# Performance work log

Hardware: AMD Instinct MI355X
Metric: run time of the kernel (lower is better)

## Reference

```python
import jax, jax.numpy as jnp
import numpy as np
import math

B, L, D, H = 16, 512, 128, 8


def setup_inputs() -> dict:
    key = jax.random.key(0)
    ks = jax.random.split(key, 10)
    xavier = lambda k, shp: jax.random.normal(k, shp, jnp.float32) * math.sqrt(2.0 / (shp[0] + shp[1]))
    inp = {
        "x": jax.random.normal(ks[0], (B, L, D), jnp.float32),
        "W_q": xavier(ks[1], (H * D, D)),
        "b_q": jnp.zeros((H * D,), jnp.float32),
        "W_k": xavier(ks[2], (H * D, D)),
        "b_k": jnp.zeros((H * D,), jnp.float32),
        "W_v": xavier(ks[3], (H * D, D)),
        "b_v": jnp.zeros((H * D,), jnp.float32),
        "W_o": xavier(ks[4], (D, H * D)),
        "b_o": jnp.zeros((D,), jnp.float32),
        "pad_mask": jax.random.randint(ks[5], (B, L, L), 0, 2).astype(bool),
        "batch_size": B,
        "max_len": L,
    }
    return inp


def reference(x, W_q, b_q, W_k, b_k, W_v, b_v, W_o, b_o, pad_mask, batch_size, max_len):
    # project: [B, L, D] -> [B, L, H*D] -> head-major [H*B, L, D]
    def proj(W, b):
        y = jnp.einsum('bld,ed->ble', x, W) + b          # [B, L, H*D]
        y = y.reshape(batch_size, max_len, H, D)
        return y.transpose(2, 0, 1, 3).reshape(H * batch_size, max_len, D)

    q = proj(W_q, b_q)
    k = proj(W_k, b_k)
    v = proj(W_v, b_v)

    scores = jnp.einsum('nqd,nkd->nqk', q, k)            # [H*B, L, L]
    mask = jnp.tile(pad_mask, (H, 1, 1))                 # repeat(n_heads,1,1)
    # faithful quirk: mask BEFORE scaling, softmax over QUERY axis (dim=1)
    scores = jnp.where(mask, -1e9, scores) / math.sqrt(D)
    attn = jax.nn.softmax(scores, axis=1)
    att = jnp.einsum('nqk,nkd->nqd', attn, v)            # [H*B, L, D]
    # faithful quirk: torch .view from (H*B, L, D) to (B, L, H*D)
    att = att.reshape(batch_size, max_len, H * D)
    out = jnp.einsum('ble,de->bld', att, W_o) + b_o      # [B, L, D]
    return out
```

## Files before the change

### kernel.cpp

```cpp
#include <hip/hip_runtime.h>

#define B_  16
#define L_  512
#define D_  128
#define H_  8
#define HD_ 1024
#define NH_ 128
#define M_  8192

typedef unsigned short u16;
typedef __attribute__((ext_vector_type(8))) short s16x8;
typedef __attribute__((ext_vector_type(4))) float f32x4;
typedef __attribute__((ext_vector_type(4))) unsigned u32x4;

__device__ __forceinline__ float bf2f(u16 u) {
    union { unsigned u; float f; } x; x.u = ((unsigned)u) << 16; return x.f;
}
__device__ __forceinline__ u16 f2bf(float f) {
    unsigned u = __float_as_uint(f);
    return (u16)((u + 0x7FFFu + ((u >> 16) & 1u)) >> 16);
}

__device__ __forceinline__ void mfma_bt64(const u16* __restrict__ A, int lda,
                                          const u16* __restrict__ B, int ldb,
                                          int K, int lane, f32x4 acc[4][4]) {
    const int mr = lane & 15, quad = lane >> 4;
    for (int k0 = 0; k0 < K; k0 += 32) {
        s16x8 av[4], bv[4];
#pragma unroll
        for (int i = 0; i < 4; i++)
            av[i] = *(const s16x8*)(A + (size_t)(i * 16 + mr) * lda + k0 + quad * 8);
#pragma unroll
        for (int j = 0; j < 4; j++)
            bv[j] = *(const s16x8*)(B + (size_t)(j * 16 + mr) * ldb + k0 + quad * 8);
#pragma unroll
        for (int i = 0; i < 4; i++)
#pragma unroll
            for (int j = 0; j < 4; j++)
                acc[i][j] = __builtin_amdgcn_mfma_f32_16x16x32_bf16(av[i], bv[j], acc[i][j], 0, 0, 0);
    }
}

__global__ void k0_detect(const unsigned int* __restrict__ pad,
                          const unsigned int* __restrict__ xw,
                          int* __restrict__ flags) {
    __shared__ int sMask, sCnt;
    if (threadIdx.x == 0) { sMask = 0; sCnt = 0; }
    __syncthreads();
    int bad = 0;
#pragma unroll
    for (int i = 0; i < 4; i++) {
        unsigned u = pad[threadIdx.x * 4 + i];
        bad |= (u > 1u) ? 1 : 0;
    }
    int cnt = 0;
#pragma unroll
    for (int i = 0; i < 16; i++) {
        unsigned w = xw[threadIdx.x * 16 + i];
        unsigned e = (w >> 7) & 0xFFu;
        cnt += (e >= 100u && e <= 131u) ? 1 : 0;
    }
    if (bad) atomicOr(&sMask, 1);
    atomicAdd(&sCnt, cnt);
    __syncthreads();
    if (threadIdx.x == 0) {
        flags[0] = (sCnt > 2048) ? 1 : 0;
        flags[1] = sMask;
    }
}

#define PREP_TOT 1576064
#define PREP_V   197008
#define PREP_CONV_BLOCKS 770
#define PREP_MASK_BLOCKS 512
__global__ __launch_bounds__(256) void kprep(
    const void* x, const void* Wq, const void* bq, const void* Wk, const void* bk,
    const void* Wv, const void* bv, const void* Wo, const void* bo,
    const void* __restrict__ pad, const int* __restrict__ flags,
    u16* xb, u16* Wqb, u16* Wkb, u16* Wvb, u16* Wob,
    u16* bqb, u16* bkb, u16* bvb, u16* bob,
    unsigned* __restrict__ mb, float* __restrict__ colsum) {
    const int b = blockIdx.x;
    if (b < PREP_CONV_BLOCKS) {
        int gid = b * 256 + threadIdx.x;
        if (gid >= PREP_V) return;
        int e0 = gid * 8;
        const int dt = flags[0];
        const void* src; u16* dst; int off;
        if      (e0 < 1048576) { src = x;  dst = xb;  off = e0; }
        else if (e0 < 1179648) { src = Wq; dst = Wqb; off = e0 - 1048576; }
        else if (e0 < 1310720) { src = Wk; dst = Wkb; off = e0 - 1179648; }
        else if (e0 < 1441792) { src = Wv; dst = Wvb; off = e0 - 1310720; }
        else if (e0 < 1572864) { src = Wo; dst = Wob; off = e0 - 1441792; }
        else if (e0 < 1573888) { src = bq; dst = bqb; off = e0 - 1572864; }
        else if (e0 < 1574912) { src = bk; dst = bkb; off = e0 - 1573888; }
        else if (e0 < 1575936) { src = bv; dst = bvb; off = e0 - 1574912; }
        else                   { src = bo; dst = bob; off = e0 - 1575936; }
        if (dt) {
            u32x4 v = __builtin_nontemporal_load((const u32x4*)((const u16*)src + off));
            *(u32x4*)(dst + off) = v;
        } else {
            const float* s = (const float*)src + off;
            f32x4 a = __builtin_nontemporal_load((const f32x4*)s);
            f32x4 c = __builtin_nontemporal_load((const f32x4*)(s + 4));
            u16 tmp[8] = {f2bf(a[0]), f2bf(a[1]), f2bf(a[2]), f2bf(a[3]),
                          f2bf(c[0]), f2bf(c[1]), f2bf(c[2]), f2bf(c[3])};
            *(u32x4*)(dst + off) = *(const u32x4*)tmp;
        }
    } else {
        int w = (b - PREP_CONV_BLOCKS) * 256 + threadIdx.x;
        if (w < NH_ * L_) colsum[w] = 0.0f;
        unsigned m = 0;
        if (flags[1]) {
            const u32x4* p = (const u32x4*)pad + (size_t)w * 2;
            u32x4 a = __builtin_nontemporal_load(p);
            u32x4 c = __builtin_nontemporal_load(p + 1);
            unsigned ws[8] = {a[0], a[1], a[2], a[3], c[0], c[1], c[2], c[3]};
#pragma unroll
            for (int i = 0; i < 8; i++) {
                unsigned v = ws[i];
                m |= ((v & 0xFFu)        ? 1u : 0u) << (i * 4)
                   | ((v & 0xFF00u)     ? 1u : 0u) << (i * 4 + 1)
                   | ((v & 0xFF0000u)   ? 1u : 0u) << (i * 4 + 2)
                   | ((v & 0xFF000000u) ? 1u : 0u) << (i * 4 + 3);
            }
        } else {
            const u32x4* p = (const u32x4*)pad + (size_t)w * 8;
#pragma unroll
            for (int i = 0; i < 8; i++) {
                u32x4 v = __builtin_nontemporal_load(p + i);
                m |= (v[0] ? 1u : 0u) << (i * 4)
                   | (v[1] ? 1u : 0u) << (i * 4 + 1)
                   | (v[2] ? 1u : 0u) << (i * 4 + 2)
                   | (v[3] ? 1u : 0u) << (i * 4 + 3);
            }
        }
        mb[w] = m;
    }
}

__global__ __launch_bounds__(256) void k1_proj(
    const u16* __restrict__ xb,
    const u16* __restrict__ Wqb, const u16* __restrict__ Wkb, const u16* __restrict__ Wvb,
    const u16* __restrict__ bqb, const u16* __restrict__ bkb, const u16* __restrict__ bvb,
    u16* __restrict__ qb, u16* __restrict__ kb, u16* __restrict__ vtb) {
    const int h  = blockIdx.y;
    const int m0 = blockIdx.x * 128;
    const int z  = blockIdx.z;
    const u16* W    = (z == 0) ? Wqb : (z == 1) ? Wkb : Wvb;
    const u16* bias = (z == 0) ? bqb : (z == 1) ? bkb : bvb;

    const int lane = threadIdx.x & 63, wave = threadIdx.x >> 6;
    const int wr = wave >> 1, wc = wave & 1;
    const int mr = lane & 15, quad = lane >> 4;

    f32x4 acc[4][4];
#pragma unroll
    for (int i = 0; i < 4; i++)
#pragma unroll
        for (int j = 0; j < 4; j++) acc[i][j] = (f32x4){0.f, 0.f, 0.f, 0.f};

    mfma_bt64(xb + (size_t)(m0 + wr * 64) * D_, D_,
              W + (size_t)(h * 128 + wc * 64) * D_, D_, D_, lane, acc);

    __shared__ __align__(16) u16 T[128][144];
#pragma unroll
    for (int i = 0; i < 4; i++)
#pragma unroll
        for (int j = 0; j < 4; j++) {
            int col = wc * 64 + j * 16 + mr;
            float bv_ = bf2f(bias[h * 128 + col]);
#pragma unroll
            for (int r = 0; r < 4; r++)
                T[wr * 64 + i * 16 + quad * 4 + r][col] = f2bf(acc[i][j][r] + bv_);
        }
    __syncthreads();

    const int bb = m0 >> 9, l0 = m0 & 511;
    const int t = threadIdx.x;
    if (z < 2) {
        u16* out = z ? kb : qb;
        const int wv = t >> 6, l = t & 63;
        const int col = (l & 15) * 8;
#pragma unroll
        for (int p = 0; p < 8; p++) {
            int row = p * 16 + wv * 4 + (l >> 4);
            u16* dst = out + ((size_t)(h * B_ + bb) * L_ + l0 + row) * D_ + col;
            *(uint4*)dst = *(const uint4*)&T[row][col];
        }
    } else {
        int d = t >> 1, lc0 = (t & 1) * 64;
        u16* dst = vtb + ((size_t)(h * B_ + bb) * D_ + d) * L_ + l0 + lc0;
#pragma unroll
        for (int c = 0; c < 64; c += 8) {
            u16 tmp[8];
#pragma unroll
            for (int s = 0; s < 8; s++) tmp[s] = T[lc0 + c + s][d];
            *(uint4*)(dst + c) = *(const uint4*)tmp;
        }
    }
}

__global__ __launch_bounds__(256, 4) void k2_scores(
    const u16* __restrict__ qb, const u16* __restrict__ kb,
    const unsigned* __restrict__ mbits,
    u16* __restrict__ sb, float* __restrict__ colsum) {
    const int bid = blockIdx.y * 16 + blockIdx.x;
    const int sw  = (bid & 7) * 256 + (bid >> 3);
    const int n   = sw >> 4;
    const int qt  = (sw >> 2) & 3, kt = sw & 3;
    const int bb  = n & (B_ - 1);
    const int lane = threadIdx.x & 63, wave = threadIdx.x >> 6;
    const int wr = wave >> 1, wc = wave & 1;
    const int mr = lane & 15, quad = lane >> 4;
    const float rs = 0.08838834764831845f;

    __shared__ __align__(16) u16 T[128][136];
    __shared__ float CS[2][128];
    __shared__ unsigned MW[128][4];

    {
        int t = threadIdx.x;
        int q = t >> 1, w2 = (t & 1) * 2;
        const unsigned* src = mbits + ((size_t)(bb << 9) + qt * 128 + q) * 16 + kt * 4 + w2;
        uint2 v = *(const uint2*)src;
        MW[q][w2] = v.x; MW[q][w2 + 1] = v.y;
    }

    f32x4 acc[4][4];
#pragma unroll
    for (int i = 0; i < 4; i++)
#pragma unroll
        for (int j = 0; j < 4; j++) acc[i][j] = (f32x4){0.f, 0.f, 0.f, 0.f};

    mfma_bt64(qb + ((size_t)n * L_ + qt * 128 + wr * 64) * D_, D_,
              kb + ((size_t)n * L_ + kt * 128 + wc * 64) * D_, D_, D_, lane, acc);
    __syncthreads();

    float cs[4] = {0.f, 0.f, 0.f, 0.f};
#pragma unroll
    for (int j = 0; j < 4; j++) {
        const int wsel = wc * 2 + (j >> 1);
        const int bit  = ((j & 1) << 4) + mr;
#pragma unroll
        for (int i = 0; i < 4; i++)
#pragma unroll
            for (int r = 0; r < 4; r++) {
                int ql = wr * 64 + i * 16 + quad * 4 + r;
                unsigned w = MW[ql][wsel];
                float e = ((w >> bit) & 1u) ? 0.f : __expf(acc[i][j][r] * rs);
                cs[j] += e;
                T[ql][wc * 64 + j * 16 + mr] = f2bf(e);
            }
    }
#pragma unroll
    for (int j = 0; j < 4; j++) {
        cs[j] += __shfl_xor(cs[j], 16);
        cs[j] += __shfl_xor(cs[j], 32);
    }
    if (quad == 0) {
#pragma unroll
        for (int j = 0; j < 4; j++) CS[wr][wc * 64 + j * 16 + mr] = cs[j];
    }
    __syncthreads();
    {
        int t = threadIdx.x;
        const int col = (t & 15) * 8;
        const int rb  = t >> 4;
#pragma unroll
        for (int p = 0; p < 8; p++) {
            int row = p * 16 + rb;
            u16* dst = sb + ((size_t)n * L_ + qt * 128 + row) * L_ + kt * 128 + col;
            *(uint4*)dst = *(const uint4*)&T[row][col];
        }
    }
    if (threadIdx.x < 128)
        atomicAdd(&colsum[(size_t)n * L_ + kt * 128 + threadIdx.x],
                  CS[0][threadIdx.x] + CS[1][threadIdx.x]);
}

__global__ __launch_bounds__(256) void k4_av(
    const u16* __restrict__ sb, const u16* __restrict__ vtb,
    const float* __restrict__ colsum, u16* __restrict__ att) {
    const int bid = blockIdx.y * 4 + blockIdx.x;
    const int sw  = (bid & 7) * 64 + (bid >> 3);
    const int n   = sw >> 2;
    const int q0  = (sw & 3) * 128;
    const int lane = threadIdx.x & 63, wave = threadIdx.x >> 6;
    const int wr = wave >> 1, wc = wave & 1;
    const int mr = lane & 15, quad = lane >> 4;

    f32x4 acc[4][4];
#pragma unroll
    for (int i = 0; i < 4; i++)
#pragma unroll
        for (int j = 0; j < 4; j++) acc[i][j] = (f32x4){0.f, 0.f, 0.f, 0.f};

    const u16* A   = sb  + ((size_t)n * L_ + q0 + wr * 64) * L_;
    const u16* Bb  = vtb + ((size_t)n * D_ + wc * 64) * L_;
    const float* cs = colsum + (size_t)n * L_;

    for (int k0 = 0; k0 < L_; k0 += 32) {
        const int kk = k0 + quad * 8;
        float lv[8];
        *(float4*)&lv[0] = *(const float4*)(cs + kk);
        *(float4*)&lv[4] = *(const float4*)(cs + kk + 4);
#pragma unroll
        for (int s = 0; s < 8; s++) lv[s] = __builtin_amdgcn_rcpf(lv[s]);

        s16x8 av[4], bv[4];
#pragma unroll
        for (int i = 0; i < 4; i++)
            av[i] = *(const s16x8*)(A + (size_t)(i * 16 + mr) * L_ + kk);
#pragma unroll
        for (int j = 0; j < 4; j++)
            bv[j] = *(const s16x8*)(Bb + (size_t)(j * 16 + mr) * L_ + kk);
#pragma unroll
        for (int i = 0; i < 4; i++) {
            u16* u = (u16*)&av[i];
#pragma unroll
            for (int s = 0; s < 8; s++) u[s] = f2bf(bf2f(u[s]) * lv[s]);
        }
#pragma unroll
        for (int i = 0; i < 4; i++)
#pragma unroll
            for (int j = 0; j < 4; j++)
                acc[i][j] = __builtin_amdgcn_mfma_f32_16x16x32_bf16(av[i], bv[j], acc[i][j], 0, 0, 0);
    }

    __shared__ __align__(16) u16 T[128][136];
#pragma unroll
    for (int i = 0; i < 4; i++)
#pragma unroll
        for (int j = 0; j < 4; j++) {
            int col = wc * 64 + j * 16 + mr;
#pragma unroll
            for (int r = 0; r < 4; r++)
                T[wr * 64 + i * 16 + quad * 4 + r][col] = f2bf(acc[i][j][r]);
        }
    __syncthreads();
    {
        int t = threadIdx.x;
        const int wv = t >> 6, l = t & 63;
        const int col = (l & 15) * 8;
#pragma unroll
        for (int p = 0; p < 8; p++) {
            int row = p * 16 + wv * 4 + (l >> 4);
            u16* dst = att + ((size_t)n * L_ + q0 + row) * D_ + col;
            *(uint4*)dst = *(const uint4*)&T[row][col];
        }
    }
}

__global__ __launch_bounds__(256) void k5_out(
    const u16* __restrict__ att, const u16* __restrict__ Wob,
    const u16* __restrict__ bob, const int* __restrict__ flags,
    void* __restrict__ out) {
    const int dt = flags[0];
    const int m0 = blockIdx.x * 32;
    const int lane = threadIdx.x & 63, wave = threadIdx.x >> 6;
    const int mr = lane & 15, quad = lane >> 4;

    f32x4 acc[2][2];
#pragma unroll
    for (int i = 0; i < 2; i++)
#pragma unroll
        for (int j = 0; j < 2; j++) acc[i][j] = (f32x4){0.f, 0.f, 0.f, 0.f};

    const u16* A  = att + (size_t)m0 * HD_;
    const u16* Bw = Wob + (size_t)(wave * 32) * HD_;
    for (int k0 = 0; k0 < HD_; k0 += 32) {
        s16x8 av[2], bv[2];
#pragma unroll
        for (int i = 0; i < 2; i++)
            av[i] = *(const s16x8*)(A + (size_t)(i * 16 + mr) * HD_ + k0 + quad * 8);
#pragma unroll
        for (int j = 0; j < 2; j++)
            bv[j] = *(const s16x8*)(Bw + (size_t)(j * 16 + mr) * HD_ + k0 + quad * 8);
#pragma unroll
        for (int i = 0; i < 2; i++)
#pragma unroll
            for (int j = 0; j < 2; j++)
                acc[i][j] = __builtin_amdgcn_mfma_f32_16x16x32_bf16(av[i], bv[j], acc[i][j], 0, 0, 0);
    }

    __shared__ __align__(16) float Tf[32][132];
#pragma unroll
    for (int i = 0; i < 2; i++)
#pragma unroll
        for (int j = 0; j < 2; j++) {
            int col = wave * 32 + j * 16 + mr;
            float bv_ = bf2f(bob[col]);
#pragma unroll
            for (int r = 0; r < 4; r++)
                Tf[i * 16 + quad * 4 + r][col] = acc[i][j][r] + bv_;
        }
    __syncthreads();
    int t = threadIdx.x, row = t >> 3, cg = (t & 7) * 16;
    size_t base = (size_t)(m0 + row) * D_ + cg;
    if (dt) {
        u16* o = (u16*)out;
        u16 tmp[16];
#pragma unroll
        for (int s = 0; s < 16; s++) tmp[s] = f2bf(Tf[row][cg + s]);
        *(uint4*)(o + base)     = *(const uint4*)&tmp[0];
        *(uint4*)(o + base + 8) = *(const uint4*)&tmp[8];
    } else {
        float* o = (float*)out;
#pragma unroll
        for (int c = 0; c < 16; c += 4)
            *(float4*)(o + base + c) = *(const float4*)&Tf[row][cg + c];
    }
}

extern "C" void kernel_launch(void* const* d_in, const int* in_sizes, int n_in,
                              void* d_out, int out_size, void* d_ws, size_t ws_size,
                              hipStream_t stream) {
    (void)in_sizes; (void)n_in; (void)out_size; (void)ws_size;
    const void* x  = d_in[0];
    const void* Wq = d_in[1]; const void* bq = d_in[2];
    const void* Wk = d_in[3]; const void* bk = d_in[4];
    const void* Wv = d_in[5]; const void* bv = d_in[6];
    const void* Wo = d_in[7]; const void* bo = d_in[8];
    const void* pad = d_in[9];

    char* p = (char*)d_ws;
    auto alloc = [&](size_t bytes) { char* r = p; p += (bytes + 255) & ~(size_t)255; return r; };
    int*  flags = (int*)alloc(256);
    u16*  xb   = (u16*)alloc(2097152);
    u16*  Wqb  = (u16*)alloc(262144);
    u16*  Wkb  = (u16*)alloc(262144);
    u16*  Wvb  = (u16*)alloc(262144);
    u16*  Wob  = (u16*)alloc(262144);
    u16*  bqb  = (u16*)alloc(2048);
    u16*  bkb  = (u16*)alloc(2048);
    u16*  bvb  = (u16*)alloc(2048);
    u16*  bob  = (u16*)alloc(256);
    unsigned* mbits = (unsigned*)alloc(524288);
    float* colsum = (float*)alloc(262144);
    u16*  qb   = (u16*)alloc(16777216);
    u16*  kb   = (u16*)alloc(16777216);
    u16*  vtb  = (u16*)alloc(16777216);
    u16*  sb   = (u16*)alloc(67108864);
    u16*  att  = qb;

    k0_detect<<<1, 256, 0, stream>>>((const unsigned*)pad, (const unsigned*)x, flags);
    kprep<<<PREP_CONV_BLOCKS + PREP_MASK_BLOCKS, 256, 0, stream>>>(
        x, Wq, bq, Wk, bk, Wv, bv, Wo, bo, pad, flags,
        xb, Wqb, Wkb, Wvb, Wob, bqb, bkb, bvb, bob, mbits, colsum);
    k1_proj<<<dim3(64, 8, 3), 256, 0, stream>>>(
        xb, Wqb, Wkb, Wvb, bqb, bkb, bvb, qb, kb, vtb);
    k2_scores<<<dim3(16, NH_), 256, 0, stream>>>(qb, kb, mbits, sb, colsum);
    k4_av<<<dim3(4, NH_), 256, 0, stream>>>(sb, vtb, colsum, att);
    k5_out<<<256, 256, 0, stream>>>(att, Wob, bob, flags, d_out);
}
```

Before: 231.5 us.

## Infer dtypes from input sizes on host and halve k2 score tile rows

The host now derives the input and mask dtypes from in_sizes and passes them as kernel arguments, so the k0_detect launch and the device flag reads are skipped when the sizes match. k2_scores switches from 128x128 to 64x128 tiles with an inline MFMA loop, which doubles the grid to 4096 blocks and halves LDS and accumulator registers per block. The intent is to drop one serial kernel launch and raise occupancy and parallelism in the scores stage, at the cost of reloading K tiles more often.

```diff
diff --git a/kernel.cpp b/kernel.cpp
--- a/kernel.cpp
+++ b/kernel.cpp
@@ -77,6 +77,7 @@
     const void* x, const void* Wq, const void* bq, const void* Wk, const void* bk,
     const void* Wv, const void* bv, const void* Wo, const void* bo,
     const void* __restrict__ pad, const int* __restrict__ flags,
+    int dth, int dtm,
     u16* xb, u16* Wqb, u16* Wkb, u16* Wvb, u16* Wob,
     u16* bqb, u16* bkb, u16* bvb, u16* bob,
     unsigned* __restrict__ mb, float* __restrict__ colsum) {
@@ -85,7 +86,7 @@
         int gid = b * 256 + threadIdx.x;
         if (gid >= PREP_V) return;
         int e0 = gid * 8;
-        const int dt = flags[0];
+        const int dt = (dth >= 0) ? dth : flags[0];
         const void* src; u16* dst; int off;
         if      (e0 < 1048576) { src = x;  dst = xb;  off = e0; }
         else if (e0 < 1179648) { src = Wq; dst = Wqb; off = e0 - 1048576; }
@@ -110,8 +111,9 @@
     } else {
         int w = (b - PREP_CONV_BLOCKS) * 256 + threadIdx.x;
         if (w < NH_ * L_) colsum[w] = 0.0f;
+        const int m8 = (dtm >= 0) ? dtm : flags[1];
         unsigned m = 0;
-        if (flags[1]) {
+        if (m8) {
             const u32x4* p = (const u32x4*)pad + (size_t)w * 2;
             u32x4 a = __builtin_nontemporal_load(p);
             u32x4 c = __builtin_nontemporal_load(p + 1);
@@ -205,36 +207,49 @@
     const u16* __restrict__ qb, const u16* __restrict__ kb,
     const unsigned* __restrict__ mbits,
     u16* __restrict__ sb, float* __restrict__ colsum) {
-    const int bid = blockIdx.y * 16 + blockIdx.x;
-    const int sw  = (bid & 7) * 256 + (bid >> 3);
-    const int n   = sw >> 4;
-    const int qt  = (sw >> 2) & 3, kt = sw & 3;
+    const int bid = blockIdx.y * 32 + blockIdx.x;
+    const int sw  = (bid & 7) * 512 + (bid >> 3);
+    const int n   = sw >> 5;
+    const int qt  = (sw >> 2) & 7, kt = sw & 3;
     const int bb  = n & (B_ - 1);
     const int lane = threadIdx.x & 63, wave = threadIdx.x >> 6;
     const int wr = wave >> 1, wc = wave & 1;
     const int mr = lane & 15, quad = lane >> 4;
     const float rs = 0.08838834764831845f;
 
-    __shared__ __align__(16) u16 T[128][136];
+    __shared__ __align__(16) u16 T[64][136];
     __shared__ float CS[2][128];
-    __shared__ unsigned MW[128][4];
+    __shared__ unsigned MW[64][4];
 
     {
         int t = threadIdx.x;
-        int q = t >> 1, w2 = (t & 1) * 2;
-        const unsigned* src = mbits + ((size_t)(bb << 9) + qt * 128 + q) * 16 + kt * 4 + w2;
-        uint2 v = *(const uint2*)src;
-        MW[q][w2] = v.x; MW[q][w2 + 1] = v.y;
-    }
-
-    f32x4 acc[4][4];
-#pragma unroll
-    for (int i = 0; i < 4; i++)
+        int q = t >> 2, w = t & 3;
+        MW[q][w] = mbits[((size_t)(bb << 9) + qt * 64 + q) * 16 + kt * 4 + w];
+    }
+
+    f32x4 acc[2][4];
+#pragma unroll
+    for (int i = 0; i < 2; i++)
 #pragma unroll
         for (int j = 0; j < 4; j++) acc[i][j] = (f32x4){0.f, 0.f, 0.f, 0.f};
 
-    mfma_bt64(qb + ((size_t)n * L_ + qt * 128 + wr * 64) * D_, D_,
-              kb + ((size_t)n * L_ + kt * 128 + wc * 64) * D_, D_, D_, lane, acc);
+    const u16* A  = qb + ((size_t)n * L_ + qt * 64 + wr * 32) * D_;
+    const u16* Bb = kb + ((size_t)n * L_ + kt * 128 + wc * 64) * D_;
+#pragma unroll
+    for (int k0 = 0; k0 < D_; k0 += 32) {
+        s16x8 av[2], bv[4];
+#pragma unroll
+        for (int i = 0; i < 2; i++)
+            av[i] = *(const s16x8*)(A + (size_t)(i * 16 + mr) * D_ + k0 + quad * 8);
+#pragma unroll
+        for (int j = 0; j < 4; j++)
+            bv[j] = *(const s16x8*)(Bb + (size_t)(j * 16 + mr) * D_ + k0 + quad * 8);
+#pragma unroll
+        for (int i = 0; i < 2; i++)
+#pragma unroll
+            for (int j = 0; j < 4; j++)
+                acc[i][j] = __builtin_amdgcn_mfma_f32_16x16x32_bf16(av[i], bv[j], acc[i][j], 0, 0, 0);
+    }
     __syncthreads();
 
     float cs[4] = {0.f, 0.f, 0.f, 0.f};
@@ -243,10 +258,10 @@
         const int wsel = wc * 2 + (j >> 1);
         const int bit  = ((j & 1) << 4) + mr;
 #pragma unroll
-        for (int i = 0; i < 4; i++)
+        for (int i = 0; i < 2; i++)
 #pragma unroll
             for (int r = 0; r < 4; r++) {
-                int ql = wr * 64 + i * 16 + quad * 4 + r;
+                int ql = wr * 32 + i * 16 + quad * 4 + r;
                 unsigned w = MW[ql][wsel];
                 float e = ((w >> bit) & 1u) ? 0.f : __expf(acc[i][j][r] * rs);
                 cs[j] += e;
@@ -268,9 +283,9 @@
         const int col = (t & 15) * 8;
         const int rb  = t >> 4;
 #pragma unroll
-        for (int p = 0; p < 8; p++) {
+        for (int p = 0; p < 4; p++) {
             int row = p * 16 + rb;
-            u16* dst = sb + ((size_t)n * L_ + qt * 128 + row) * L_ + kt * 128 + col;
+            u16* dst = sb + ((size_t)n * L_ + qt * 64 + row) * L_ + kt * 128 + col;
             *(uint4*)dst = *(const uint4*)&T[row][col];
         }
     }
@@ -354,9 +369,9 @@
 
 __global__ __launch_bounds__(256) void k5_out(
     const u16* __restrict__ att, const u16* __restrict__ Wob,
-    const u16* __restrict__ bob, const int* __restrict__ flags,
+    const u16* __restrict__ bob, const int* __restrict__ flags, int dth,
     void* __restrict__ out) {
-    const int dt = flags[0];
+    const int dt = (dth >= 0) ? dth : flags[0];
     const int m0 = blockIdx.x * 32;
     const int lane = threadIdx.x & 63, wave = threadIdx.x >> 6;
     const int mr = lane & 15, quad = lane >> 4;
@@ -416,7 +431,7 @@
 extern "C" void kernel_launch(void* const* d_in, const int* in_sizes, int n_in,
                               void* d_out, int out_size, void* d_ws, size_t ws_size,
                               hipStream_t stream) {
-    (void)in_sizes; (void)n_in; (void)out_size; (void)ws_size;
+    (void)out_size; (void)ws_size;
     const void* x  = d_in[0];
     const void* Wq = d_in[1]; const void* bq = d_in[2];
     const void* Wk = d_in[3]; const void* bk = d_in[4];
@@ -444,13 +459,26 @@
     u16*  sb   = (u16*)alloc(67108864);
     u16*  att  = qb;
 
-    k0_detect<<<1, 256, 0, stream>>>((const unsigned*)pad, (const unsigned*)x, flags);
+    int dth = -1, dtm = -1;
+    if (in_sizes && n_in >= 10) {
+        if      (in_sizes[0] == 4194304) dth = 0;
+        else if (in_sizes[0] == 2097152) dth = 1;
+        if (dth >= 0) {
+            if      (in_sizes[9] == 16777216) dtm = 0;
+            else if (in_sizes[9] == 4194304)  dtm = 1;
+        }
+    }
+    if (dth < 0 || dtm < 0) {
+        dth = -1; dtm = -1;
+        k0_detect<<<1, 256, 0, stream>>>((const unsigned*)pad, (const unsigned*)x, flags);
+    }
+
     kprep<<<PREP_CONV_BLOCKS + PREP_MASK_BLOCKS, 256, 0, stream>>>(
-        x, Wq, bq, Wk, bk, Wv, bv, Wo, bo, pad, flags,
+        x, Wq, bq, Wk, bk, Wv, bv, Wo, bo, pad, flags, dth, dtm,
         xb, Wqb, Wkb, Wvb, Wob, bqb, bkb, bvb, bob, mbits, colsum);
     k1_proj<<<dim3(64, 8, 3), 256, 0, stream>>>(
         xb, Wqb, Wkb, Wvb, bqb, bkb, bvb, qb, kb, vtb);
-    k2_scores<<<dim3(16, NH_), 256, 0, stream>>>(qb, kb, mbits, sb, colsum);
+    k2_scores<<<dim3(32, NH_), 256, 0, stream>>>(qb, kb, mbits, sb, colsum);
     k4_av<<<dim3(4, NH_), 256, 0, stream>>>(sb, vtb, colsum, att);
-    k5_out<<<256, 256, 0, stream>>>(att, Wob, bob, flags, d_out);
-}
+    k5_out<<<256, 256, 0, stream>>>(att, Wob, bob, flags, dth, d_out);
+}
```

After: 235.0 us. Within noise of the previous version (+1.5%).

## Fuse input bf16 conversion and mask packing into projection kernel

Applied to the files above, without the earlier changes.

Removes the separate prep kernel that converted x and the weights to bf16. The projection and output kernels now load fp32 (or bf16) inputs directly and convert fragments in registers. Mask bit-packing and colsum zeroing move into an extra z-slice of the projection grid. The dtype is inferred from in_sizes on the host so the detect kernel can be skipped. This saves two launches and a round-trip of converted data through memory, at the cost of redundant conversions: each x and W element is re-converted by every block that reads it, and fp32 loads are twice as wide.

```diff
diff --git a/kernel.cpp b/kernel.cpp
--- a/kernel.cpp
+++ b/kernel.cpp
@@ -21,23 +21,17 @@
     return (u16)((u + 0x7FFFu + ((u >> 16) & 1u)) >> 16);
 }
 
-__device__ __forceinline__ void mfma_bt64(const u16* __restrict__ A, int lda,
-                                          const u16* __restrict__ B, int ldb,
-                                          int K, int lane, f32x4 acc[4][4]) {
-    const int mr = lane & 15, quad = lane >> 4;
-    for (int k0 = 0; k0 < K; k0 += 32) {
-        s16x8 av[4], bv[4];
-#pragma unroll
-        for (int i = 0; i < 4; i++)
-            av[i] = *(const s16x8*)(A + (size_t)(i * 16 + mr) * lda + k0 + quad * 8);
-#pragma unroll
-        for (int j = 0; j < 4; j++)
-            bv[j] = *(const s16x8*)(B + (size_t)(j * 16 + mr) * ldb + k0 + quad * 8);
-#pragma unroll
-        for (int i = 0; i < 4; i++)
-#pragma unroll
-            for (int j = 0; j < 4; j++)
-                acc[i][j] = __builtin_amdgcn_mfma_f32_16x16x32_bf16(av[i], bv[j], acc[i][j], 0, 0, 0);
+__device__ __forceinline__ s16x8 ldfrag8(const void* __restrict__ base,
+                                         size_t off, int dt) {
+    if (dt) {
+        return *(const s16x8*)((const u16*)base + off);
+    } else {
+        const float* s = (const float*)base + off;
+        f32x4 a = *(const f32x4*)s;
+        f32x4 b = *(const f32x4*)(s + 4);
+        u16 tmp[8] = {f2bf(a[0]), f2bf(a[1]), f2bf(a[2]), f2bf(a[3]),
+                      f2bf(b[0]), f2bf(b[1]), f2bf(b[2]), f2bf(b[3])};
+        return *(const s16x8*)tmp;
     }
 }
 
@@ -69,49 +63,20 @@
     }
 }
 
-#define PREP_TOT 1576064
-#define PREP_V   197008
-#define PREP_CONV_BLOCKS 770
-#define PREP_MASK_BLOCKS 512
-__global__ __launch_bounds__(256) void kprep(
-    const void* x, const void* Wq, const void* bq, const void* Wk, const void* bk,
-    const void* Wv, const void* bv, const void* Wo, const void* bo,
+__global__ __launch_bounds__(256) void k1_proj(
+    const void* __restrict__ x,
+    const void* __restrict__ Wq, const void* __restrict__ Wk, const void* __restrict__ Wv,
+    const void* __restrict__ bq, const void* __restrict__ bk, const void* __restrict__ bv,
     const void* __restrict__ pad, const int* __restrict__ flags,
-    u16* xb, u16* Wqb, u16* Wkb, u16* Wvb, u16* Wob,
-    u16* bqb, u16* bkb, u16* bvb, u16* bob,
+    int dth, int dtm,
+    u16* __restrict__ qb, u16* __restrict__ kb, u16* __restrict__ vtb,
     unsigned* __restrict__ mb, float* __restrict__ colsum) {
-    const int b = blockIdx.x;
-    if (b < PREP_CONV_BLOCKS) {
-        int gid = b * 256 + threadIdx.x;
-        if (gid >= PREP_V) return;
-        int e0 = gid * 8;
-        const int dt = flags[0];
-        const void* src; u16* dst; int off;
-        if      (e0 < 1048576) { src = x;  dst = xb;  off = e0; }
-        else if (e0 < 1179648) { src = Wq; dst = Wqb; off = e0 - 1048576; }
-        else if (e0 < 1310720) { src = Wk; dst = Wkb; off = e0 - 1179648; }
-        else if (e0 < 1441792) { src = Wv; dst = Wvb; off = e0 - 1310720; }
-        else if (e0 < 1572864) { src = Wo; dst = Wob; off = e0 - 1441792; }
-        else if (e0 < 1573888) { src = bq; dst = bqb; off = e0 - 1572864; }
-        else if (e0 < 1574912) { src = bk; dst = bkb; off = e0 - 1573888; }
-        else if (e0 < 1575936) { src = bv; dst = bvb; off = e0 - 1574912; }
-        else                   { src = bo; dst = bob; off = e0 - 1575936; }
-        if (dt) {
-            u32x4 v = __builtin_nontemporal_load((const u32x4*)((const u16*)src + off));
-            *(u32x4*)(dst + off) = v;
-        } else {
-            const float* s = (const float*)src + off;
-            f32x4 a = __builtin_nontemporal_load((const f32x4*)s);
-            f32x4 c = __builtin_nontemporal_load((const f32x4*)(s + 4));
-            u16 tmp[8] = {f2bf(a[0]), f2bf(a[1]), f2bf(a[2]), f2bf(a[3]),
-                          f2bf(c[0]), f2bf(c[1]), f2bf(c[2]), f2bf(c[3])};
-            *(u32x4*)(dst + off) = *(const u32x4*)tmp;
-        }
-    } else {
-        int w = (b - PREP_CONV_BLOCKS) * 256 + threadIdx.x;
+    if (blockIdx.z == 3) {
+        int w = (blockIdx.y * 64 + blockIdx.x) * 256 + threadIdx.x;
         if (w < NH_ * L_) colsum[w] = 0.0f;
+        const int m8 = (dtm >= 0) ? dtm : flags[1];
         unsigned m = 0;
-        if (flags[1]) {
+        if (m8) {
             const u32x4* p = (const u32x4*)pad + (size_t)w * 2;
             u32x4 a = __builtin_nontemporal_load(p);
             u32x4 c = __builtin_nontemporal_load(p + 1);
@@ -136,19 +101,15 @@
             }
         }
         mb[w] = m;
-    }
-}
-
-__global__ __launch_bounds__(256) void k1_proj(
-    const u16* __restrict__ xb,
-    const u16* __restrict__ Wqb, const u16* __restrict__ Wkb, const u16* __restrict__ Wvb,
-    const u16* __restrict__ bqb, const u16* __restrict__ bkb, const u16* __restrict__ bvb,
-    u16* __restrict__ qb, u16* __restrict__ kb, u16* __restrict__ vtb) {
+        return;
+    }
+
+    const int dt = (dth >= 0) ? dth : flags[0];
     const int h  = blockIdx.y;
     const int m0 = blockIdx.x * 128;
     const int z  = blockIdx.z;
-    const u16* W    = (z == 0) ? Wqb : (z == 1) ? Wkb : Wvb;
-    const u16* bias = (z == 0) ? bqb : (z == 1) ? bkb : bvb;
+    const void* W    = (z == 0) ? Wq : (z == 1) ? Wk : Wv;
+    const void* bias = (z == 0) ? bq : (z == 1) ? bk : bv;
 
     const int lane = threadIdx.x & 63, wave = threadIdx.x >> 6;
     const int wr = wave >> 1, wc = wave & 1;
@@ -160,8 +121,20 @@
 #pragma unroll
         for (int j = 0; j < 4; j++) acc[i][j] = (f32x4){0.f, 0.f, 0.f, 0.f};
 
-    mfma_bt64(xb + (size_t)(m0 + wr * 64) * D_, D_,
-              W + (size_t)(h * 128 + wc * 64) * D_, D_, D_, lane, acc);
+    for (int k0 = 0; k0 < D_; k0 += 32) {
+        s16x8 av[4], bvf[4];
+#pragma unroll
+        for (int i = 0; i < 4; i++)
+            av[i] = ldfrag8(x, (size_t)(m0 + wr * 64 + i * 16 + mr) * D_ + k0 + quad * 8, dt);
+#pragma unroll
+        for (int j = 0; j < 4; j++)
+            bvf[j] = ldfrag8(W, (size_t)(h * 128 + wc * 64 + j * 16 + mr) * D_ + k0 + quad * 8, dt);
+#pragma unroll
+        for (int i = 0; i < 4; i++)
+#pragma unroll
+            for (int j = 0; j < 4; j++)
+                acc[i][j] = __builtin_amdgcn_mfma_f32_16x16x32_bf16(av[i], bvf[j], acc[i][j], 0, 0, 0);
+    }
 
     __shared__ __align__(16) u16 T[128][144];
 #pragma unroll
@@ -169,7 +142,8 @@
 #pragma unroll
         for (int j = 0; j < 4; j++) {
             int col = wc * 64 + j * 16 + mr;
-            float bv_ = bf2f(bias[h * 128 + col]);
+            float bv_ = dt ? bf2f(((const u16*)bias)[h * 128 + col])
+                           : ((const float*)bias)[h * 128 + col];
 #pragma unroll
             for (int r = 0; r < 4; r++)
                 T[wr * 64 + i * 16 + quad * 4 + r][col] = f2bf(acc[i][j][r] + bv_);
@@ -233,8 +207,24 @@
 #pragma unroll
         for (int j = 0; j < 4; j++) acc[i][j] = (f32x4){0.f, 0.f, 0.f, 0.f};
 
-    mfma_bt64(qb + ((size_t)n * L_ + qt * 128 + wr * 64) * D_, D_,
-              kb + ((size_t)n * L_ + kt * 128 + wc * 64) * D_, D_, D_, lane, acc);
+    {
+        const u16* A  = qb + ((size_t)n * L_ + qt * 128 + wr * 64) * D_;
+        const u16* Bb = kb + ((size_t)n * L_ + kt * 128 + wc * 64) * D_;
+        for (int k0 = 0; k0 < D_; k0 += 32) {
+            s16x8 av[4], bv[4];
+#pragma unroll
+            for (int i = 0; i < 4; i++)
+                av[i] = *(const s16x8*)(A + (size_t)(i * 16 + mr) * D_ + k0 + quad * 8);
+#pragma unroll
+            for (int j = 0; j < 4; j++)
+                bv[j] = *(const s16x8*)(Bb + (size_t)(j * 16 + mr) * D_ + k0 + quad * 8);
+#pragma unroll
+            for (int i = 0; i < 4; i++)
+#pragma unroll
+                for (int j = 0; j < 4; j++)
+                    acc[i][j] = __builtin_amdgcn_mfma_f32_16x16x32_bf16(av[i], bv[j], acc[i][j], 0, 0, 0);
+        }
+    }
     __syncthreads();
 
     float cs[4] = {0.f, 0.f, 0.f, 0.f};
@@ -353,10 +343,10 @@
 }
 
 __global__ __launch_bounds__(256) void k5_out(
-    const u16* __restrict__ att, const u16* __restrict__ Wob,
-    const u16* __restrict__ bob, const int* __restrict__ flags,
+    const u16* __restrict__ att, const void* __restrict__ Wo,
+    const void* __restrict__ bo, const int* __restrict__ flags, int dth,
     void* __restrict__ out) {
-    const int dt = flags[0];
+    const int dt = (dth >= 0) ? dth : flags[0];
     const int m0 = blockIdx.x * 32;
     const int lane = threadIdx.x & 63, wave = threadIdx.x >> 6;
     const int mr = lane & 15, quad = lane >> 4;
@@ -367,8 +357,7 @@
 #pragma unroll
         for (int j = 0; j < 2; j++) acc[i][j] = (f32x4){0.f, 0.f, 0.f, 0.f};
 
-    const u16* A  = att + (size_t)m0 * HD_;
-    const u16* Bw = Wob + (size_t)(wave * 32) * HD_;
+    const u16* A = att + (size_t)m0 * HD_;
     for (int k0 = 0; k0 < HD_; k0 += 32) {
         s16x8 av[2], bv[2];
 #pragma unroll
@@ -376,7 +365,7 @@
             av[i] = *(const s16x8*)(A + (size_t)(i * 16 + mr) * HD_ + k0 + quad * 8);
 #pragma unroll
         for (int j = 0; j < 2; j++)
-            bv[j] = *(const s16x8*)(Bw + (size_t)(j * 16 + mr) * HD_ + k0 + quad * 8);
+            bv[j] = ldfrag8(Wo, (size_t)(wave * 32 + j * 16 + mr) * HD_ + k0 + quad * 8, dt);
 #pragma unroll
         for (int i = 0; i < 2; i++)
 #pragma unroll
@@ -390,7 +379,7 @@
 #pragma unroll
         for (int j = 0; j < 2; j++) {
             int col = wave * 32 + j * 16 + mr;
-            float bv_ = bf2f(bob[col]);
+            float bv_ = dt ? bf2f(((const u16*)bo)[col]) : ((const float*)bo)[col];
 #pragma unroll
             for (int r = 0; r < 4; r++)
                 Tf[i * 16 + quad * 4 + r][col] = acc[i][j][r] + bv_;
@@ -416,7 +405,7 @@
 extern "C" void kernel_launch(void* const* d_in, const int* in_sizes, int n_in,
                               void* d_out, int out_size, void* d_ws, size_t ws_size,
                               hipStream_t stream) {
-    (void)in_sizes; (void)n_in; (void)out_size; (void)ws_size;
+    (void)out_size; (void)ws_size;
     const void* x  = d_in[0];
     const void* Wq = d_in[1]; const void* bq = d_in[2];
     const void* Wk = d_in[3]; const void* bk = d_in[4];
@@ -427,15 +416,6 @@
     char* p = (char*)d_ws;
     auto alloc = [&](size_t bytes) { char* r = p; p += (bytes + 255) & ~(size_t)255; return r; };
     int*  flags = (int*)alloc(256);
-    u16*  xb   = (u16*)alloc(2097152);
-    u16*  Wqb  = (u16*)alloc(262144);
-    u16*  Wkb  = (u16*)alloc(262144);
-    u16*  Wvb  = (u16*)alloc(262144);
-    u16*  Wob  = (u16*)alloc(262144);
-    u16*  bqb  = (u16*)alloc(2048);
-    u16*  bkb  = (u16*)alloc(2048);
-    u16*  bvb  = (u16*)alloc(2048);
-    u16*  bob  = (u16*)alloc(256);
     unsigned* mbits = (unsigned*)alloc(524288);
     float* colsum = (float*)alloc(262144);
     u16*  qb   = (u16*)alloc(16777216);
@@ -444,13 +424,24 @@
     u16*  sb   = (u16*)alloc(67108864);
     u16*  att  = qb;
 
-    k0_detect<<<1, 256, 0, stream>>>((const unsigned*)pad, (const unsigned*)x, flags);
-    kprep<<<PREP_CONV_BLOCKS + PREP_MASK_BLOCKS, 256, 0, stream>>>(
-        x, Wq, bq, Wk, bk, Wv, bv, Wo, bo, pad, flags,
-        xb, Wqb, Wkb, Wvb, Wob, bqb, bkb, bvb, bob, mbits, colsum);
-    k1_proj<<<dim3(64, 8, 3), 256, 0, stream>>>(
-        xb, Wqb, Wkb, Wvb, bqb, bkb, bvb, qb, kb, vtb);
+    int dth = -1, dtm = -1;
+    if (in_sizes && n_in >= 10) {
+        if      (in_sizes[0] == 4194304) dth = 0;
+        else if (in_sizes[0] == 2097152) dth = 1;
+        if (dth >= 0) {
+            if      (in_sizes[9] == 16777216) dtm = 0;
+            else if (in_sizes[9] == 4194304)  dtm = 1;
+        }
+    }
+    if (dth < 0 || dtm < 0) {
+        dth = -1; dtm = -1;
+        k0_detect<<<1, 256, 0, stream>>>((const unsigned*)pad, (const unsigned*)x, flags);
+    }
+
+    k1_proj<<<dim3(64, 8, 4), 256, 0, stream>>>(
+        x, Wq, Wk, Wv, bq, bk, bv, pad, flags, dth, dtm,
+        qb, kb, vtb, mbits, colsum);
     k2_scores<<<dim3(16, NH_), 256, 0, stream>>>(qb, kb, mbits, sb, colsum);
     k4_av<<<dim3(4, NH_), 256, 0, stream>>>(sb, vtb, colsum, att);
-    k5_out<<<256, 256, 0, stream>>>(att, Wob, bob, flags, d_out);
-}
+    k5_out<<<256, 256, 0, stream>>>(att, Wo, bo, flags, dth, d_out);
+}
```

After: 288.0 us. 24.4% more time.
